# Performance work log

Hardware: AMD Instinct MI355X
Metric: run time of the kernel (lower is better)

Reference implementation:

```python
import jax, jax.numpy as jnp
import numpy as np

B, D_IN, H, HV, A, E, HW = 16384, 512, 512, 256, 32, 8, 512

def _lin(key, fan_in, fan_out):
    k1, k2 = jax.random.split(key)
    s = 1.0 / np.sqrt(fan_in)
    W = jax.random.uniform(k1, (fan_in, fan_out), minval=-s, maxval=s, dtype=jnp.float32)
    b = jax.random.uniform(k2, (fan_out,), minval=-s, maxval=s, dtype=jnp.float32)
    return W, b

def _stack(key, n, fan_in, fan_out):
    Ws, bs = [], []
    for k in jax.random.split(key, n):
        W, b = _lin(k, fan_in, fan_out)
        Ws.append(W); bs.append(b)
    return jnp.stack(Ws), jnp.stack(bs)

def setup_inputs() -> dict:
    key = jax.random.key(0)
    ks = jax.random.split(key, 16)
    x = jax.random.normal(ks[0], (B, D_IN), dtype=jnp.float32)
    # stacked expert policy nets: in->H, H->H, H->A (tanh)
    Wp0, bp0 = _stack(ks[1], E, D_IN, H)
    Wp1, bp1 = _stack(ks[2], E, H, H)
    Wmu, bmu = _stack(ks[3], E, H, A)
    # stacked expert value nets (hardcoded 256 hidden in source): in->256, 256->256, 256->1
    Wv0, bv0 = _stack(ks[4], E, D_IN, HV)
    Wv1, bv1 = _stack(ks[5], E, HV, HV)
    Wv, bv = _stack(ks[6], E, HV, 1)
    # gating net: in->HW, HW->HW, HW->E, softmax
    Ww0, bw0 = _lin(ks[7], D_IN, HW)
    Ww1, bw1 = _lin(ks[8], HW, HW)
    Wwo, bwo = _lin(ks[9], HW, E)
    return dict(x=x, Wp0=Wp0, bp0=bp0, Wp1=Wp1, bp1=bp1, Wmu=Wmu, bmu=bmu,
                Wv0=Wv0, bv0=bv0, Wv1=Wv1, bv1=bv1, Wv=Wv, bv=bv,
                Ww0=Ww0, bw0=bw0, Ww1=Ww1, bw1=bw1, Wwo=Wwo, bwo=bwo)

def reference(x, Wp0, bp0, Wp1, bp1, Wmu, bmu, Wv0, bv0, Wv1, bv1, Wv, bv,
              Ww0, bw0, Ww1, bw1, Wwo, bwo):
    # experts as one grouped/batched GEMM over axis e
    h = jax.nn.relu(jnp.einsum('bi,eih->ebh', x, Wp0) + bp0[:, None, :])      # [E,B,H]
    h = jax.nn.relu(jnp.einsum('ebh,ehk->ebk', h, Wp1) + bp1[:, None, :])
    actions = jnp.tanh(jnp.einsum('ebh,eha->eba', h, Wmu) + bmu[:, None, :])  # [E,B,A]
    # per-expert values
    g = jax.nn.relu(jnp.einsum('bi,eih->ebh', x, Wv0) + bv0[:, None, :])      # [E,B,HV]
    g = jax.nn.relu(jnp.einsum('ebh,ehk->ebk', g, Wv1) + bv1[:, None, :])
    values = jnp.einsum('ebh,eho->ebo', g, Wv) + bv[:, None, :]               # [E,B,1]
    # gating network + softmax
    u = jax.nn.relu(x @ Ww0 + bw0)
    u = jax.nn.relu(u @ Ww1 + bw1)
    w = jax.nn.softmax(u @ Wwo + bwo, axis=-1)                                # [B,E]
    # Categorical(w).sample() with a fixed key, then per-row gather of values
    pis = jax.random.categorical(jax.random.key(42), jnp.log(w), axis=-1)     # [B] int
    v = values[pis, jnp.arange(values.shape[1])]                              # [B,1]
    return actions, v, w
```

## Files before the change

kernel.cpp:

```cpp
#include <hip/hip_runtime.h>


typedef float   f32x4 __attribute__((ext_vector_type(4)));
typedef _Float16 f16;
typedef _Float16 f16x4 __attribute__((ext_vector_type(4)));
typedef _Float16 f16x8 __attribute__((ext_vector_type(8)));

typedef __attribute__((address_space(1))) unsigned int gas_u32;
typedef __attribute__((address_space(3))) unsigned int las_u32;

__device__ __forceinline__ void gl_lds16(const void* g, void* l) {
  __builtin_amdgcn_global_load_lds((gas_u32*)g, (las_u32*)l, 16, 0, 0);
}

__device__ __forceinline__ int xcd_swz(int b, int G) {
  int q = G >> 3, r = G & 7;
  int x = b & 7, y = b >> 3;
  return (x < r ? x * (q + 1) : r * (q + 1) + (x - r) * q) + y;
}

template<int EPI>
__global__ __launch_bounds__(512, 4) void gemm3_kernel(
    const f16* __restrict__ A, const f16* __restrict__ BT,
    const float* __restrict__ bias, void* __restrict__ Cv,
    const int K, const int lda, const int ldc,
    const long long sAe, const long long sCe,
    const int mT, const int nInner, const int eShift,
    const float* __restrict__ Wv, float* __restrict__ values)
{
  constexpr int BM = 256, BN = 128;
  __shared__ __align__(16) char sm[(BM + BN) * 128];
  char* Ash = sm;
  char* Bsh = sm + BM * 128;

  const int tid = threadIdx.x;
  const int lane = tid & 63;
  const int wid = tid >> 6;
  const int wr = wid >> 1, wc = wid & 1;

  const int L = xcd_swz(blockIdx.x, gridDim.x);
  const int nIn = L % nInner;
  const int m = (L / nInner) % mT;
  const int eo = L / (nInner * mT);
  const int nv0 = (eo * nInner + nIn) * BN;
  const int e = nv0 >> eShift;
  const int col0 = nv0 & ((1 << eShift) - 1);
  const int m0 = m * BM;

  const f16* Ab = A + (size_t)sAe * e + (size_t)m0 * lda;
  const f16* Bb = BT + (size_t)nv0 * K;

  f32x4 acc[4][4] = {};
  const int ksteps = K >> 6;

  for (int kt = 0; kt < ksteps; ++kt) {
    __syncthreads();
    const f16* Ak = Ab + (kt << 6);
    const f16* Bk = Bb + (kt << 6);
    #pragma unroll
    for (int u0 = 0; u0 < BM * 8; u0 += 512) {
      int u = u0 + tid;
      int row = u >> 3;
      int kb = ((u & 7) << 4) ^ ((row & 7) << 4);
      gl_lds16(Ak + (size_t)row * lda + (kb >> 1), Ash + u * 16);
    }
    #pragma unroll
    for (int u0 = 0; u0 < BN * 8; u0 += 512) {
      int u = u0 + tid;
      int row = u >> 3;
      int kb = ((u & 7) << 4) ^ ((row & 7) << 4);
      gl_lds16(Bk + (size_t)row * K + (kb >> 1), Bsh + u * 16);
    }
    __syncthreads();

    f16x8 af[4][2], bf[4][2];
    const int kl = (lane >> 4) << 4;
    #pragma unroll
    for (int fm = 0; fm < 4; ++fm) {
      int row = wr * 64 + fm * 16 + (lane & 15);
      int sw = (row & 7) << 4;
      af[fm][0] = *(const f16x8*)(Ash + row * 128 + (kl ^ sw));
      af[fm][1] = *(const f16x8*)(Ash + row * 128 + ((64 + kl) ^ sw));
    }
    #pragma unroll
    for (int fn = 0; fn < 4; ++fn) {
      int row = wc * 64 + fn * 16 + (lane & 15);
      int sw = (row & 7) << 4;
      bf[fn][0] = *(const f16x8*)(Bsh + row * 128 + (kl ^ sw));
      bf[fn][1] = *(const f16x8*)(Bsh + row * 128 + ((64 + kl) ^ sw));
    }
    #pragma unroll
    for (int fm = 0; fm < 4; ++fm)
      #pragma unroll
      for (int fn = 0; fn < 4; ++fn) {
        acc[fm][fn] = __builtin_amdgcn_mfma_f32_16x16x32_f16(
            bf[fn][0], af[fm][0], acc[fm][fn], 0, 0, 0);
        acc[fm][fn] = __builtin_amdgcn_mfma_f32_16x16x32_f16(
            bf[fn][1], af[fm][1], acc[fm][fn], 0, 0, 0);
      }
  }

  const int rbase = m0 + wr * 64 + (lane & 15);
  const int cb = wc * 64 + ((lane >> 4) << 2);

  if constexpr (EPI == 4) {
    #pragma unroll
    for (int fm = 0; fm < 4; ++fm) {
      const int row = rbase + fm * 16;
      float s = 0.0f;
      #pragma unroll
      for (int fn = 0; fn < 4; ++fn) {
        const int bcol = cb + fn * 16;
        const int col = col0 + bcol;
        f32x4 v = acc[fm][fn];
        f32x4 bb = *(const f32x4*)(bias + nv0 + bcol);
        #pragma unroll
        for (int r = 0; r < 4; ++r)
          s += fmaxf(v[r] + bb[r], 0.0f) * Wv[(e << 8) + col + r];
      }
      s += __shfl_xor(s, 16);
      s += __shfl_xor(s, 32);
      if (lane < 16) atomicAdd(&values[((size_t)e << 14) + row], s);
    }
    return;
  }

  #pragma unroll
  for (int fm = 0; fm < 4; ++fm) {
    const int row = rbase + fm * 16;
    #pragma unroll
    for (int fn = 0; fn < 4; ++fn) {
      const int bcol = cb + fn * 16;
      const int col = col0 + bcol;
      f32x4 v = acc[fm][fn];
      f32x4 bb = *(const f32x4*)(bias + nv0 + bcol);
      f16x4 h;
      #pragma unroll
      for (int r = 0; r < 4; ++r) h[r] = (f16)fmaxf(v[r] + bb[r], 0.0f);
      *(f16x4*)((f16*)Cv + (size_t)sCe * e + (size_t)row * ldc + col) = h;
    }
  }
}

template<int BM, int BN, int WM, int WN, int EPI>
__global__ __launch_bounds__(256, 2) void gemm2_kernel(
    const f16* __restrict__ A, const f16* __restrict__ BT,
    const float* __restrict__ bias, void* __restrict__ Cv,
    const int K, const int lda, const int ldc,
    const long long sAe, const long long sCe,
    const int mT, const int nInner, const int eShift)
{
  constexpr int FM = WM / 16, FN = WN / 16;
  constexpr int WAVES_N = BN / WN;
  __shared__ __align__(16) char sm[(BM + BN) * 128];
  char* Ash = sm;
  char* Bsh = sm + BM * 128;

  const int tid = threadIdx.x;
  const int lane = tid & 63;
  const int wid = tid >> 6;

  const int L = xcd_swz(blockIdx.x, gridDim.x);
  const int nIn = L % nInner;
  const int m = (L / nInner) % mT;
  const int eo = L / (nInner * mT);
  const int nv0 = (eo * nInner + nIn) * BN;
  const int e = nv0 >> eShift;
  const int col0 = nv0 & ((1 << eShift) - 1);
  const int m0 = m * BM;

  const f16* Ab = A + (size_t)sAe * e + (size_t)m0 * lda;
  const f16* Bb = BT + (size_t)nv0 * K;
  const int wr = wid / WAVES_N, wc = wid % WAVES_N;

  f32x4 acc[FM][FN] = {};
  const int ksteps = K >> 6;

  for (int kt = 0; kt < ksteps; ++kt) {
    __syncthreads();
    const f16* Ak = Ab + (kt << 6);
    const f16* Bk = Bb + (kt << 6);
    for (int u0 = 0; u0 < BM * 8; u0 += 256) {
      int u = u0 + tid;
      int row = u >> 3;
      int kb = ((u & 7) << 4) ^ ((row & 7) << 4);
      gl_lds16(Ak + (size_t)row * lda + (kb >> 1), Ash + u * 16);
    }
    for (int u0 = 0; u0 < BN * 8; u0 += 256) {
      int u = u0 + tid;
      int row = u >> 3;
      int kb = ((u & 7) << 4) ^ ((row & 7) << 4);
      gl_lds16(Bk + (size_t)row * K + (kb >> 1), Bsh + u * 16);
    }
    __syncthreads();

    f16x8 af[FM][2], bf[FN][2];
    const int kl = (lane >> 4) << 4;
    #pragma unroll
    for (int fm = 0; fm < FM; ++fm) {
      int row = wr * WM + fm * 16 + (lane & 15);
      int sw = (row & 7) << 4;
      af[fm][0] = *(const f16x8*)(Ash + row * 128 + (kl ^ sw));
      af[fm][1] = *(const f16x8*)(Ash + row * 128 + ((64 + kl) ^ sw));
    }
    #pragma unroll
    for (int fn = 0; fn < FN; ++fn) {
      int row = wc * WN + fn * 16 + (lane & 15);
      int sw = (row & 7) << 4;
      bf[fn][0] = *(const f16x8*)(Bsh + row * 128 + (kl ^ sw));
      bf[fn][1] = *(const f16x8*)(Bsh + row * 128 + ((64 + kl) ^ sw));
    }
    #pragma unroll
    for (int fm = 0; fm < FM; ++fm)
      #pragma unroll
      for (int fn = 0; fn < FN; ++fn) {
        acc[fm][fn] = __builtin_amdgcn_mfma_f32_16x16x32_f16(
            bf[fn][0], af[fm][0], acc[fm][fn], 0, 0, 0);
        acc[fm][fn] = __builtin_amdgcn_mfma_f32_16x16x32_f16(
            bf[fn][1], af[fm][1], acc[fm][fn], 0, 0, 0);
      }
  }

  const int rbase = m0 + wr * WM + (lane & 15);
  const int cb = wc * WN + ((lane >> 4) << 2);
  #pragma unroll
  for (int fm = 0; fm < FM; ++fm) {
    const int row = rbase + fm * 16;
    #pragma unroll
    for (int fn = 0; fn < FN; ++fn) {
      const int bcol = cb + fn * 16;
      const int col = col0 + bcol;
      f32x4 v = acc[fm][fn];
      f32x4 bb = *(const f32x4*)(bias + nv0 + bcol);
      if constexpr (EPI == 1) {
        f32x4 o;
        #pragma unroll
        for (int r = 0; r < 4; ++r) o[r] = tanhf(v[r] + bb[r]);
        *(f32x4*)((float*)Cv + (size_t)sCe * e + (size_t)row * ldc + col) = o;
      } else if constexpr (EPI == 2) {
        f32x4 o;
        #pragma unroll
        for (int r = 0; r < 4; ++r) o[r] = fmaxf(v[r] + bb[r], 0.0f);
        *(f32x4*)((float*)Cv + (size_t)sCe * e + (size_t)row * ldc + col) = o;
      } else {
        f16x4 h, l, s;
        #pragma unroll
        for (int r = 0; r < 4; ++r) {
          float u = fmaxf(v[r] + bb[r], 0.0f);
          f16 hh = (f16)u;
          float hv = (float)hh;
          h[r] = hh;
          l[r] = (f16)((u - hv) * 32.0f);
          s[r] = (f16)(hv * 0.03125f);
        }
        f16* cp = (f16*)Cv + (size_t)sCe * e + (size_t)row * ldc + col;
        *(f16x4*)(cp) = h;
        *(f16x4*)(cp + 512) = l;
        *(f16x4*)(cp + 1024) = s;
      }
    }
  }
}

__global__ __launch_bounds__(256) void prep_kernel(
    const float* __restrict__ x, f16* __restrict__ xsplit,
    const float* __restrict__ Wp0, f16* __restrict__ Wp0T,
    const float* __restrict__ Wp1, f16* __restrict__ Wp1T,
    const float* __restrict__ Wmu, f16* __restrict__ WmuT,
    const float* __restrict__ Wv0, f16* __restrict__ Wv0T,
    const float* __restrict__ Wv1, f16* __restrict__ Wv1T,
    const float* __restrict__ Ww0, f16* __restrict__ Ww0T3,
    const float* __restrict__ Ww1, f16* __restrict__ Ww1T3)
{
  __shared__ float t[32][33];
  const int tid = threadIdx.x;
  int b = blockIdx.x;
  if (b < 8192) {
    const size_t i = ((size_t)b * 256 + tid) * 4;
    const int row = (int)(i >> 9);
    const int col = (int)(i & 511);
    f32x4 v = *(const f32x4*)(x + i);
    f16x4 h, l, s;
    #pragma unroll
    for (int j = 0; j < 4; ++j) {
      f16 hh = (f16)v[j];
      float hv = (float)hh;
      h[j] = hh;
      l[j] = (f16)((v[j] - hv) * 32.0f);
      s[j] = (f16)(hv * 0.03125f);
    }
    f16* p = xsplit + (size_t)row * 1536 + col;
    *(f16x4*)(p) = h;
    *(f16x4*)(p + 512) = l;
    *(f16x4*)(p + 1024) = s;
    return;
  }
  b -= 8192;
  const float* W;
  f16* T;
  bool triple = false;
  int K, N;
  if (b < 2048)               { W = Wp0; T = Wp0T; K = 512; N = 512; }
  else if ((b -= 2048) < 2048){ W = Wp1; T = Wp1T; K = 512; N = 512; }
  else if ((b -= 2048) < 128) { W = Wmu; T = WmuT; K = 512; N = 32; }
  else if ((b -= 128) < 1024) { W = Wv0; T = Wv0T; K = 512; N = 256; }
  else if ((b -= 1024) < 512) { W = Wv1; T = Wv1T; K = 256; N = 256; }
  else if ((b -= 512) < 256)  { W = Ww0; T = Ww0T3; triple = true; K = 512; N = 512; }
  else { b -= 256;              W = Ww1; T = Ww1T3; triple = true; K = 512; N = 512; }

  const int kT = K >> 5, nT = N >> 5;
  const int e = b / (kT * nT);
  const int rem = b % (kT * nT);
  const int k0 = (rem % kT) << 5;
  const int n0 = (rem / kT) << 5;
  const int tx = tid & 31, ty = tid >> 5;
  const float* Wp = W + (size_t)e * K * N;
  #pragma unroll
  for (int i = 0; i < 4; ++i)
    t[ty + i * 8][tx] = Wp[(size_t)(k0 + ty + i * 8) * N + n0 + tx];
  __syncthreads();
  #pragma unroll
  for (int i = 0; i < 4; ++i) {
    const int n = n0 + ty + i * 8, k = k0 + tx;
    float v = t[tx][ty + i * 8];
    f16 hh = (f16)v;
    if (!triple) {
      T[(size_t)e * K * N + (size_t)n * K + k] = hh;
    } else {
      float hv = (float)hh;
      f16* p = T + (size_t)n * 1536 + k;
      p[0] = hh;
      p[512] = (f16)(hv * 0.03125f);
      p[1024] = (f16)((v - hv) * 32.0f);
    }
  }
}

__device__ __forceinline__ void threefry_0_42(unsigned x0, unsigned x1,
                                              unsigned& o0, unsigned& o1)
{
  const unsigned ks0 = 0u, ks1 = 42u, ks2 = 0x1BD11BDAu ^ 42u;
  x0 += ks0; x1 += ks1;
#define TF_R(r) { x0 += x1; x1 = (x1 << r) | (x1 >> (32 - r)); x1 ^= x0; }
  TF_R(13) TF_R(15) TF_R(26) TF_R(6)  x0 += ks1; x1 += ks2 + 1u;
  TF_R(17) TF_R(29) TF_R(16) TF_R(24) x0 += ks2; x1 += ks0 + 2u;
  TF_R(13) TF_R(15) TF_R(26) TF_R(6)  x0 += ks0; x1 += ks1 + 3u;
  TF_R(17) TF_R(29) TF_R(16) TF_R(24) x0 += ks1; x1 += ks2 + 4u;
  TF_R(13) TF_R(15) TF_R(26) TF_R(6)  x0 += ks2; x1 += ks0 + 5u;
#undef TF_R
  o0 = x0; o1 = x1;
}

__global__ __launch_bounds__(256) void gating_out_kernel(
    const float* __restrict__ U2, const float* __restrict__ Wwo,
    const float* __restrict__ bwo, const float* __restrict__ values,
    const float* __restrict__ bv,
    float* __restrict__ w_out, float* __restrict__ v_out)
{
  __shared__ float wl[4096];
  const int tid = threadIdx.x;
  for (int i = tid; i < 1024; i += 256)
    ((f32x4*)wl)[i] = ((const f32x4*)Wwo)[i];
  __syncthreads();
  const int lane = tid & 63, wid = tid >> 6;
  const int b = blockIdx.x * 4 + wid;

  const float* u = U2 + (size_t)b * 512 + lane * 8;
  f32x4 ua = *(const f32x4*)u;
  f32x4 ub = *(const f32x4*)(u + 4);
  float acc[8] = {};
  const float* wrow = wl + lane * 64;
  #pragma unroll
  for (int i = 0; i < 8; ++i) {
    float uv = (i < 4) ? ua[i] : ub[i - 4];
    #pragma unroll
    for (int ee = 0; ee < 8; ++ee) acc[ee] += uv * wrow[i * 8 + ee];
  }
  #pragma unroll
  for (int off = 32; off >= 1; off >>= 1)
    #pragma unroll
    for (int ee = 0; ee < 8; ++ee) acc[ee] += __shfl_xor(acc[ee], off);
  #pragma unroll
  for (int ee = 0; ee < 8; ++ee) acc[ee] += bwo[ee];

  float zmax = acc[0];
  #pragma unroll
  for (int ee = 1; ee < 8; ++ee) zmax = fmaxf(zmax, acc[ee]);
  float s = 0.0f;
  #pragma unroll
  for (int ee = 0; ee < 8; ++ee) s += expf(acc[ee] - zmax);

  float t0 = (lane & 1) ? acc[1] : acc[0];
  float t1 = (lane & 1) ? acc[3] : acc[2];
  float t2 = (lane & 1) ? acc[5] : acc[4];
  float t3 = (lane & 1) ? acc[7] : acc[6];
  float s0 = (lane & 2) ? t1 : t0;
  float s1 = (lane & 2) ? t3 : t2;
  float zown = (lane & 4) ? s1 : s0;

  if (lane < 8) w_out[(size_t)b * 8 + lane] = expf(zown - zmax) / s;

  unsigned idx = ((unsigned)b << 3) | (unsigned)(lane & 7);
  unsigned o0, o1;
  threefry_0_42(0u, idx, o0, o1);
  unsigned bits = o0 ^ o1;
  float f = __uint_as_float((bits >> 9) | 0x3F800000u) - 1.0f;
  f = fmaxf(f, 1.17549435e-38f);
  float g = -logf(-logf(f));
  float y = (lane < 8) ? (zown + g) : -3.0e38f;

  float best = __shfl(y, 0);
  int pi = 0;
  #pragma unroll
  for (int ee = 1; ee < 8; ++ee) {
    float ye = __shfl(y, ee);
    if (ye > best) { best = ye; pi = ee; }
  }
  if (lane == 0) v_out[b] = values[((size_t)pi << 14) + b] + bv[pi];
}

extern "C" void kernel_launch(void* const* d_in, const int* in_sizes, int n_in,
                              void* d_out, int out_size, void* d_ws, size_t ws_size,
                              hipStream_t stream) {
  (void)in_sizes; (void)n_in; (void)out_size; (void)ws_size;
  const float* x   = (const float*)d_in[0];
  const float* Wp0 = (const float*)d_in[1];
  const float* bp0 = (const float*)d_in[2];
  const float* Wp1 = (const float*)d_in[3];
  const float* bp1 = (const float*)d_in[4];
  const float* Wmu = (const float*)d_in[5];
  const float* bmu = (const float*)d_in[6];
  const float* Wv0 = (const float*)d_in[7];
  const float* bv0 = (const float*)d_in[8];
  const float* Wv1 = (const float*)d_in[9];
  const float* bv1 = (const float*)d_in[10];
  const float* Wv  = (const float*)d_in[11];
  const float* bv  = (const float*)d_in[12];
  const float* Ww0 = (const float*)d_in[13];
  const float* bw0 = (const float*)d_in[14];
  const float* Ww1 = (const float*)d_in[15];
  const float* bw1 = (const float*)d_in[16];
  const float* Wwo = (const float*)d_in[17];
  const float* bwo = (const float*)d_in[18];

  float* out_actions = (float*)d_out;
  float* out_v = out_actions + (size_t)8 * 16384 * 32;
  float* out_w = out_v + 16384;

  char* base = (char*)d_ws;
  size_t off = 0;
  auto alloc = [&](size_t bytes) -> char* {
    char* p = base + off;
    off = (off + bytes + 255) & ~(size_t)255;
    return p;
  };

  f16* xsplit = (f16*)alloc((size_t)16384 * 1536 * 2);
  f16* Wp0T   = (f16*)alloc((size_t)8 * 512 * 512 * 2);
  f16* Wp1T   = (f16*)alloc((size_t)8 * 512 * 512 * 2);
  f16* WmuT   = (f16*)alloc((size_t)8 * 32 * 512 * 2);
  f16* Wv0T   = (f16*)alloc((size_t)8 * 256 * 512 * 2);
  f16* Wv1T   = (f16*)alloc((size_t)8 * 256 * 256 * 2);
  f16* Ww0T3  = (f16*)alloc((size_t)512 * 1536 * 2);
  f16* Ww1T3  = (f16*)alloc((size_t)512 * 1536 * 2);
  float* valuesBuf = (float*)alloc((size_t)8 * 16384 * 4);

  char* arena = base + off;
  const size_t SZ67 = (size_t)67108864;
  f16* P1 = (f16*)arena;
  f16* P2 = (f16*)(arena + SZ67);
  f16* VB1 = (f16*)arena;
  f16* U1split = (f16*)arena;
  float* U2 = (float*)(arena + (size_t)50331648);

  dim3 blk(256);
  dim3 blk8(512);
  const long long sBD = 16384LL * 512;
  const long long sBH = 16384LL * 256;

  prep_kernel<<<14464, blk, 0, stream>>>(
      x, xsplit, Wp0, Wp0T, Wp1, Wp1T, Wmu, WmuT, Wv0, Wv0T, Wv1, Wv1T,
      Ww0, Ww0T3, Ww1, Ww1T3);

  for (int e0 = 0; e0 < 8; e0 += 4) {
    gemm3_kernel<0><<<1024, blk8, 0, stream>>>(
        xsplit, Wp0T + (size_t)e0 * 512 * 512, bp0 + e0 * 512, P1,
        512, 1536, 512, 0, sBD, 64, 16, 9, nullptr, nullptr);
    gemm3_kernel<0><<<1024, blk8, 0, stream>>>(
        P1, Wp1T + (size_t)e0 * 512 * 512, bp1 + e0 * 512, P2,
        512, 512, 512, sBD, sBD, 64, 4, 9, nullptr, nullptr);
    gemm2_kernel<128, 32, 32, 32, 1><<<512, blk, 0, stream>>>(
        P2, WmuT + (size_t)e0 * 32 * 512, bmu + e0 * 32,
        out_actions + (size_t)e0 * 16384 * 32,
        512, 512, 32, sBD, 16384LL * 32, 128, 1, 5);
  }

  gemm3_kernel<0><<<1024, blk8, 0, stream>>>(
      xsplit, Wv0T, bv0, VB1, 512, 1536, 256, 0, sBH, 64, 16, 8,
      nullptr, nullptr);
  hipMemsetAsync(valuesBuf, 0, (size_t)8 * 16384 * 4, stream);
  gemm3_kernel<4><<<1024, blk8, 0, stream>>>(
      VB1, Wv1T, bv1, nullptr, 256, 256, 256, sBH, 0, 64, 2, 8,
      Wv, valuesBuf);

  gemm2_kernel<128, 128, 64, 64, 3><<<512, blk, 0, stream>>>(
      xsplit, Ww0T3, bw0, U1split, 1536, 1536, 1536, 0, 0, 128, 4, 9);
  gemm2_kernel<128, 128, 64, 64, 2><<<512, blk, 0, stream>>>(
      U1split, Ww1T3, bw1, U2, 1536, 1536, 512, 0, 0, 128, 4, 9);
  gating_out_kernel<<<4096, blk, 0, stream>>>(
      U2, Wwo, bwo, valuesBuf, bv, out_w, out_v);
}
```

Before: 426.0 us.

## Fuse gating output projection into second gating GEMM epilogue with atomics

The second gating GEMM epilogue now applies ReLU, multiplies by Wwo and accumulates the 8 logits per row into a zero-initialised buffer with atomicAdd. This removes the fp32 U2 intermediate write and re-read. A slimmer tail kernel then does softmax, sampling and the value gather, one row per 8 lanes. The gating GEMMs also move to 128x64 tiles with twice as many blocks, and the memsets are merged into one at the start. The cost is many global atomics and per-element Wwo loads in the epilogue, and the float atomic sums are non-deterministic, which could flip a near-tie in the sampled expert.

```diff
diff --git a/kernel.cpp b/kernel.cpp
--- a/kernel.cpp
+++ b/kernel.cpp
@@ -148,7 +148,8 @@
     const float* __restrict__ bias, void* __restrict__ Cv,
     const int K, const int lda, const int ldc,
     const long long sAe, const long long sCe,
-    const int mT, const int nInner, const int eShift)
+    const int mT, const int nInner, const int eShift,
+    const float* __restrict__ Wwo, float* __restrict__ zbuf)
 {
   constexpr int FM = WM / 16, FN = WN / 16;
   constexpr int WAVES_N = BN / WN;
@@ -223,6 +224,40 @@
 
   const int rbase = m0 + wr * WM + (lane & 15);
   const int cb = wc * WN + ((lane >> 4) << 2);
+
+  if constexpr (EPI == 5) {
+    #pragma unroll
+    for (int fm = 0; fm < FM; ++fm) {
+      const int row = rbase + fm * 16;
+      float s[8] = {};
+      #pragma unroll
+      for (int fn = 0; fn < FN; ++fn) {
+        const int bcol = cb + fn * 16;
+        const int col = col0 + bcol;
+        f32x4 v = acc[fm][fn];
+        f32x4 bb = *(const f32x4*)(bias + nv0 + bcol);
+        #pragma unroll
+        for (int r = 0; r < 4; ++r) {
+          float u = fmaxf(v[r] + bb[r], 0.0f);
+          const float* wp = Wwo + (size_t)(col + r) * 8;
+          #pragma unroll
+          for (int ee = 0; ee < 8; ++ee) s[ee] += u * wp[ee];
+        }
+      }
+      #pragma unroll
+      for (int ee = 0; ee < 8; ++ee) {
+        s[ee] += __shfl_xor(s[ee], 16);
+        s[ee] += __shfl_xor(s[ee], 32);
+      }
+      if (lane < 16) {
+        #pragma unroll
+        for (int ee = 0; ee < 8; ++ee)
+          atomicAdd(&zbuf[(size_t)row * 8 + ee], s[ee]);
+      }
+    }
+    return;
+  }
+
   #pragma unroll
   for (int fm = 0; fm < FM; ++fm) {
     const int row = rbase + fm * 16;
@@ -236,11 +271,6 @@
         f32x4 o;
         #pragma unroll
         for (int r = 0; r < 4; ++r) o[r] = tanhf(v[r] + bb[r]);
-        *(f32x4*)((float*)Cv + (size_t)sCe * e + (size_t)row * ldc + col) = o;
-      } else if constexpr (EPI == 2) {
-        f32x4 o;
-        #pragma unroll
-        for (int r = 0; r < 4; ++r) o[r] = fmaxf(v[r] + bb[r], 0.0f);
         *(f32x4*)((float*)Cv + (size_t)sCe * e + (size_t)row * ldc + col) = o;
       } else {
         f16x4 h, l, s;
@@ -351,72 +381,44 @@
   o0 = x0; o1 = x1;
 }
 
-__global__ __launch_bounds__(256) void gating_out_kernel(
-    const float* __restrict__ U2, const float* __restrict__ Wwo,
-    const float* __restrict__ bwo, const float* __restrict__ values,
-    const float* __restrict__ bv,
+__global__ __launch_bounds__(256) void tail_kernel(
+    const float* __restrict__ zbuf, const float* __restrict__ bwo,
+    const float* __restrict__ values, const float* __restrict__ bv,
     float* __restrict__ w_out, float* __restrict__ v_out)
 {
-  __shared__ float wl[4096];
   const int tid = threadIdx.x;
-  for (int i = tid; i < 1024; i += 256)
-    ((f32x4*)wl)[i] = ((const f32x4*)Wwo)[i];
-  __syncthreads();
   const int lane = tid & 63, wid = tid >> 6;
-  const int b = blockIdx.x * 4 + wid;
-
-  const float* u = U2 + (size_t)b * 512 + lane * 8;
-  f32x4 ua = *(const f32x4*)u;
-  f32x4 ub = *(const f32x4*)(u + 4);
-  float acc[8] = {};
-  const float* wrow = wl + lane * 64;
-  #pragma unroll
-  for (int i = 0; i < 8; ++i) {
-    float uv = (i < 4) ? ua[i] : ub[i - 4];
-    #pragma unroll
-    for (int ee = 0; ee < 8; ++ee) acc[ee] += uv * wrow[i * 8 + ee];
-  }
-  #pragma unroll
-  for (int off = 32; off >= 1; off >>= 1)
-    #pragma unroll
-    for (int ee = 0; ee < 8; ++ee) acc[ee] += __shfl_xor(acc[ee], off);
-  #pragma unroll
-  for (int ee = 0; ee < 8; ++ee) acc[ee] += bwo[ee];
-
-  float zmax = acc[0];
-  #pragma unroll
-  for (int ee = 1; ee < 8; ++ee) zmax = fmaxf(zmax, acc[ee]);
-  float s = 0.0f;
-  #pragma unroll
-  for (int ee = 0; ee < 8; ++ee) s += expf(acc[ee] - zmax);
-
-  float t0 = (lane & 1) ? acc[1] : acc[0];
-  float t1 = (lane & 1) ? acc[3] : acc[2];
-  float t2 = (lane & 1) ? acc[5] : acc[4];
-  float t3 = (lane & 1) ? acc[7] : acc[6];
-  float s0 = (lane & 2) ? t1 : t0;
-  float s1 = (lane & 2) ? t3 : t2;
-  float zown = (lane & 4) ? s1 : s0;
-
-  if (lane < 8) w_out[(size_t)b * 8 + lane] = expf(zown - zmax) / s;
-
-  unsigned idx = ((unsigned)b << 3) | (unsigned)(lane & 7);
+  const int row = (blockIdx.x * 4 + wid) * 8 + (lane >> 3);
+  const int e = lane & 7;
+
+  float z = zbuf[(size_t)row * 8 + e] + bwo[e];
+
+  float zm = z;
+  #pragma unroll
+  for (int off = 1; off < 8; off <<= 1) zm = fmaxf(zm, __shfl_xor(zm, off));
+  float ew = expf(z - zm);
+  float s = ew;
+  #pragma unroll
+  for (int off = 1; off < 8; off <<= 1) s += __shfl_xor(s, off);
+  w_out[(size_t)row * 8 + e] = ew / s;
+
+  unsigned idx = ((unsigned)row << 3) | (unsigned)e;
   unsigned o0, o1;
   threefry_0_42(0u, idx, o0, o1);
   unsigned bits = o0 ^ o1;
   float f = __uint_as_float((bits >> 9) | 0x3F800000u) - 1.0f;
   f = fmaxf(f, 1.17549435e-38f);
   float g = -logf(-logf(f));
-  float y = (lane < 8) ? (zown + g) : -3.0e38f;
-
-  float best = __shfl(y, 0);
-  int pi = 0;
-  #pragma unroll
-  for (int ee = 1; ee < 8; ++ee) {
-    float ye = __shfl(y, ee);
-    if (ye > best) { best = ye; pi = ee; }
-  }
-  if (lane == 0) v_out[b] = values[((size_t)pi << 14) + b] + bv[pi];
+
+  float my = z + g;
+  int mi = e;
+  #pragma unroll
+  for (int off = 1; off < 8; off <<= 1) {
+    float oy = __shfl_xor(my, off);
+    int oi = __shfl_xor(mi, off);
+    if (oy > my || (oy == my && oi < mi)) { my = oy; mi = oi; }
+  }
+  if (e == 0) v_out[row] = values[((size_t)mi << 14) + row] + bv[mi];
 }
 
 extern "C" void kernel_launch(void* const* d_in, const int* in_sizes, int n_in,
@@ -464,6 +466,7 @@
   f16* Ww0T3  = (f16*)alloc((size_t)512 * 1536 * 2);
   f16* Ww1T3  = (f16*)alloc((size_t)512 * 1536 * 2);
   float* valuesBuf = (float*)alloc((size_t)8 * 16384 * 4);
+  float* zbuf      = (float*)alloc((size_t)16384 * 8 * 4);
 
   char* arena = base + off;
   const size_t SZ67 = (size_t)67108864;
@@ -471,13 +474,13 @@
   f16* P2 = (f16*)(arena + SZ67);
   f16* VB1 = (f16*)arena;
   f16* U1split = (f16*)arena;
-  float* U2 = (float*)(arena + (size_t)50331648);
 
   dim3 blk(256);
   dim3 blk8(512);
   const long long sBD = 16384LL * 512;
   const long long sBH = 16384LL * 256;
 
+  hipMemsetAsync(valuesBuf, 0, (size_t)(8 * 16384 + 16384 * 8) * 4, stream);
   prep_kernel<<<14464, blk, 0, stream>>>(
       x, xsplit, Wp0, Wp0T, Wp1, Wp1T, Wmu, WmuT, Wv0, Wv0T, Wv1, Wv1T,
       Ww0, Ww0T3, Ww1, Ww1T3);
@@ -492,21 +495,21 @@
     gemm2_kernel<128, 32, 32, 32, 1><<<512, blk, 0, stream>>>(
         P2, WmuT + (size_t)e0 * 32 * 512, bmu + e0 * 32,
         out_actions + (size_t)e0 * 16384 * 32,
-        512, 512, 32, sBD, 16384LL * 32, 128, 1, 5);
+        512, 512, 32, sBD, 16384LL * 32, 128, 1, 5, nullptr, nullptr);
   }
 
   gemm3_kernel<0><<<1024, blk8, 0, stream>>>(
       xsplit, Wv0T, bv0, VB1, 512, 1536, 256, 0, sBH, 64, 16, 8,
       nullptr, nullptr);
-  hipMemsetAsync(valuesBuf, 0, (size_t)8 * 16384 * 4, stream);
   gemm3_kernel<4><<<1024, blk8, 0, stream>>>(
       VB1, Wv1T, bv1, nullptr, 256, 256, 256, sBH, 0, 64, 2, 8,
       Wv, valuesBuf);
 
-  gemm2_kernel<128, 128, 64, 64, 3><<<512, blk, 0, stream>>>(
-      xsplit, Ww0T3, bw0, U1split, 1536, 1536, 1536, 0, 0, 128, 4, 9);
-  gemm2_kernel<128, 128, 64, 64, 2><<<512, blk, 0, stream>>>(
-      U1split, Ww1T3, bw1, U2, 1536, 1536, 512, 0, 0, 128, 4, 9);
-  gating_out_kernel<<<4096, blk, 0, stream>>>(
-      U2, Wwo, bwo, valuesBuf, bv, out_w, out_v);
-}
+  gemm2_kernel<128, 64, 64, 32, 3><<<1024, blk, 0, stream>>>(
+      xsplit, Ww0T3, bw0, U1split, 1536, 1536, 1536, 0, 0, 128, 8, 9,
+      nullptr, nullptr);
+  gemm2_kernel<128, 64, 64, 32, 5><<<1024, blk, 0, stream>>>(
+      U1split, Ww1T3, bw1, nullptr, 1536, 1536, 0, 0, 0, 128, 8, 9,
+      Wwo, zbuf);
+  tail_kernel<<<512, blk, 0, stream>>>(zbuf, bwo, valuesBuf, bv, out_w, out_v);
+}
```

After: 452.8 us. 6.3% more time.
